# Kernel optimization log

Hardware: AMD Instinct MI355X
Metric: run time of the kernel (lower is better)

Reference implementation:

```python
import jax, jax.numpy as jnp
import numpy as np

TAU_MEM = 20.0          # tau for both ExpLeak (syn) and LIF (mem)
SPIKE_THRESHOLD = 1.0
WIDTH_GRAD = 0.5        # surrogate gradient width (unused in fwd)
SCALE_GRAD = 1.0


def setup_inputs() -> dict:
    key = jax.random.key(0)
    k1, k2 = jax.random.split(key)
    x = jax.random.normal(k1, (32, 2048, 512, 1), dtype=jnp.float32)
    weight = jax.random.uniform(k2, (1, 1), dtype=jnp.float32)  # Linear(1,1,bias=False) weight (set to scalar `weight` in torch)
    return {"x": x, "weight": weight}


def reference(x, weight):
    # x: (B, T, N, 1); weight: (1, 1)
    alpha = jnp.exp(jnp.asarray(-1.0 / TAU_MEM, dtype=x.dtype))
    i_in = x * weight[0, 0]                      # Linear(1,1,no bias)
    i_in = jnp.moveaxis(i_in, 1, 0)              # (T, B, N, 1) for scan over time

    def step(carry, i_t):
        v_syn, v_mem = carry
        # ExpLeak, norm_input=False: v_syn = alpha*v_syn + input
        v_syn = alpha * v_syn + i_t
        # LIF, norm_input=False: decay then integrate synaptic current
        v_mem = alpha * v_mem + v_syn
        # SingleSpike: at most one spike per step
        spk = (v_mem >= SPIKE_THRESHOLD).astype(v_mem.dtype)
        # MembraneSubtract reset
        v_mem = v_mem - SPIKE_THRESHOLD * spk
        return (v_syn, v_mem), spk

    zeros = jnp.zeros_like(i_in[0])
    _, spikes = jax.lax.scan(step, (zeros, zeros), i_in)
    return jnp.moveaxis(spikes, 0, 1)            # (B, T, N, 1)
```

## Files before the change

### kernel.cpp

```cpp
#include <hip/hip_runtime.h>
#include <math.h>


constexpr int B_ = 32;
constexpr int T_ = 2048;
constexpr int N_ = 512;
constexpr int TILE = 32;
constexpr int NT = T_ / TILE;

__global__ __launch_bounds__(64, 1)
void exodus_direct_kernel(const float* __restrict__ x,
                          const float* __restrict__ wptr,
                          float* __restrict__ out) {
    const int blk  = blockIdx.x;
    const int b    = blk >> 3;
    const int n0   = (blk & 7) * 64;
    const int lane = threadIdx.x;

    const size_t base = (size_t)b * T_ * N_ + (size_t)n0 + lane;
    const float* __restrict__ xp = x + base;
    float* __restrict__ op = out + base;

    const float w = wptr[0];
    const float alpha = (float)exp((double)(-1.0f / 20.0f));

    float bufA[TILE], bufB[TILE];

#pragma unroll
    for (int i = 0; i < TILE; ++i) bufA[i] = xp[(size_t)i * N_];

    float vsyn = 0.0f, vmem = 0.0f;

    for (int t = 0; t < NT; t += 2) {
        {
            const float* __restrict__ g = xp + (size_t)(t + 1) * TILE * N_;
#pragma unroll
            for (int i = 0; i < TILE; ++i) bufB[i] = g[(size_t)i * N_];
        }
        {
            float* __restrict__ o = op + (size_t)t * TILE * N_;
#pragma unroll
            for (int j = 0; j < TILE; ++j) {
                const float i_t = __fmul_rn(bufA[j], w);
                vsyn = __fadd_rn(__fmul_rn(alpha, vsyn), i_t);
                const float va = __fadd_rn(__fmul_rn(alpha, vmem), vsyn);
                const bool fire = (va >= 1.0f);
                __builtin_nontemporal_store(fire ? 1.0f : 0.0f,
                                            o + (size_t)j * N_);
                vmem = fire ? __fsub_rn(va, 1.0f) : va;
            }
        }
        if (t + 2 < NT) {
            const float* __restrict__ g = xp + (size_t)(t + 2) * TILE * N_;
#pragma unroll
            for (int i = 0; i < TILE; ++i) bufA[i] = g[(size_t)i * N_];
        }
        {
            float* __restrict__ o = op + (size_t)(t + 1) * TILE * N_;
#pragma unroll
            for (int j = 0; j < TILE; ++j) {
                const float i_t = __fmul_rn(bufB[j], w);
                vsyn = __fadd_rn(__fmul_rn(alpha, vsyn), i_t);
                const float va = __fadd_rn(__fmul_rn(alpha, vmem), vsyn);
                const bool fire = (va >= 1.0f);
                __builtin_nontemporal_store(fire ? 1.0f : 0.0f,
                                            o + (size_t)j * N_);
                vmem = fire ? __fsub_rn(va, 1.0f) : va;
            }
        }
    }
}

extern "C" void kernel_launch(void* const* d_in, const int* in_sizes, int n_in,
                              void* d_out, int out_size, void* d_ws, size_t ws_size,
                              hipStream_t stream) {
    const float* x = (const float*)d_in[0];
    const float* w = (const float*)d_in[1];
    float* out = (float*)d_out;

    dim3 grid(256);
    dim3 block(64);
    hipLaunchKernelGGL(exodus_direct_kernel, grid, block, 0, stream, x, w, out);
}
```

Baseline: 258.6 us.

## Hand-schedule loads and stores with inline asm and four-deep tile prefetch

Replaces the compiler-generated double-buffered loop with inline-asm global loads and stores that use a scalar base plus lane offset. Four input tile buffers keep two tiles of prefetch in flight, and explicit s_waitcnt vmcnt counts with sched barriers control how much memory traffic stays outstanding. This targets memory latency stalls in the sequential scan, where only 256 single-wave blocks run. The cost is higher register pressure, fragile manual waitcnt accounting, and stores that are no longer nontemporal.

```diff
diff --git a/kernel.cpp b/kernel.cpp
--- a/kernel.cpp
+++ b/kernel.cpp
@@ -2,73 +2,95 @@
 #include <math.h>
 
 
-constexpr int B_ = 32;
 constexpr int T_ = 2048;
 constexpr int N_ = 512;
 constexpr int TILE = 32;
 constexpr int NT = T_ / TILE;
 
+#define GLOADTILE(BUF, TT)                                                   \
+  {                                                                          \
+    const float* gp_ = xq + (size_t)(TT) * TILE * N_;                        \
+    _Pragma("unroll")                                                        \
+    for (int i_ = 0; i_ < TILE; ++i_) {                                      \
+      asm volatile("global_load_dword %0, %1, %2"                            \
+                   : "=v"(BUF[i_])                                           \
+                   : "v"(voff), "s"(gp_ + (size_t)i_ * N_));                 \
+    }                                                                        \
+  }
+
+#define COMPUTE(BUF, SPK, TT)                                                \
+  {                                                                          \
+    const float* op_ = oq + (size_t)(TT) * TILE * N_;                        \
+    _Pragma("unroll")                                                        \
+    for (int j_ = 0; j_ < TILE; ++j_) {                                      \
+      const float it_ = __fmul_rn(BUF[j_], w);                               \
+      vsyn = __fadd_rn(__fmul_rn(alpha, vsyn), it_);                         \
+      const float va_ = __fadd_rn(__fmul_rn(alpha, vmem), vsyn);             \
+      const bool fire_ = (va_ >= 1.0f);                                      \
+      SPK[j_] = fire_ ? 1.0f : 0.0f;                                         \
+      asm volatile("global_store_dword %1, %0, %2"                           \
+                   :: "v"(SPK[j_]), "v"(voff),                               \
+                      "s"(op_ + (size_t)j_ * N_)                             \
+                   : "memory");                                              \
+      vmem = fire_ ? __fsub_rn(va_, 1.0f) : va_;                             \
+    }                                                                        \
+  }
+
+#define KEEPALIVE16(S, O)                                                    \
+  asm volatile("" :: "v"(S[(O)+0]),  "v"(S[(O)+1]),  "v"(S[(O)+2]),          \
+                     "v"(S[(O)+3]),  "v"(S[(O)+4]),  "v"(S[(O)+5]),          \
+                     "v"(S[(O)+6]),  "v"(S[(O)+7]),  "v"(S[(O)+8]),          \
+                     "v"(S[(O)+9]),  "v"(S[(O)+10]), "v"(S[(O)+11]),         \
+                     "v"(S[(O)+12]), "v"(S[(O)+13]), "v"(S[(O)+14]),         \
+                     "v"(S[(O)+15]))
+
+#define SUBSTEP(BUFC, SPKC, SPKP, BUFP, TT, DOPF)                            \
+  {                                                                          \
+    COMPUTE(BUFC, SPKC, TT);                                                 \
+    asm volatile("s_waitcnt vmcnt(32)");                                     \
+    __builtin_amdgcn_sched_barrier(0);                                       \
+    KEEPALIVE16(SPKP, 0);                                                    \
+    KEEPALIVE16(SPKP, 16);                                                   \
+    if (DOPF) { GLOADTILE(BUFP, (TT) + 2); }                                 \
+  }
+
 __global__ __launch_bounds__(64, 1)
-void exodus_direct_kernel(const float* __restrict__ x,
-                          const float* __restrict__ wptr,
-                          float* __restrict__ out) {
+void exodus_asm_kernel(const float* __restrict__ x,
+                       const float* __restrict__ wptr,
+                       float* __restrict__ out) {
     const int blk  = blockIdx.x;
     const int b    = blk >> 3;
     const int n0   = (blk & 7) * 64;
     const int lane = threadIdx.x;
 
-    const size_t base = (size_t)b * T_ * N_ + (size_t)n0 + lane;
-    const float* __restrict__ xp = x + base;
-    float* __restrict__ op = out + base;
+    const float* __restrict__ xq  = x   + (size_t)b * T_ * N_ + n0;
+    float*       __restrict__ oq  = out + (size_t)b * T_ * N_ + n0;
+    const unsigned voff = (unsigned)lane * 4u;
 
     const float w = wptr[0];
     const float alpha = (float)exp((double)(-1.0f / 20.0f));
-
-    float bufA[TILE], bufB[TILE];
-
-#pragma unroll
-    for (int i = 0; i < TILE; ++i) bufA[i] = xp[(size_t)i * N_];
-
     float vsyn = 0.0f, vmem = 0.0f;
 
-    for (int t = 0; t < NT; t += 2) {
-        {
-            const float* __restrict__ g = xp + (size_t)(t + 1) * TILE * N_;
+    float B0[TILE], B1[TILE], B2[TILE], B3[TILE];
+    float s0[TILE], s1[TILE];
 #pragma unroll
-            for (int i = 0; i < TILE; ++i) bufB[i] = g[(size_t)i * N_];
-        }
-        {
-            float* __restrict__ o = op + (size_t)t * TILE * N_;
-#pragma unroll
-            for (int j = 0; j < TILE; ++j) {
-                const float i_t = __fmul_rn(bufA[j], w);
-                vsyn = __fadd_rn(__fmul_rn(alpha, vsyn), i_t);
-                const float va = __fadd_rn(__fmul_rn(alpha, vmem), vsyn);
-                const bool fire = (va >= 1.0f);
-                __builtin_nontemporal_store(fire ? 1.0f : 0.0f,
-                                            o + (size_t)j * N_);
-                vmem = fire ? __fsub_rn(va, 1.0f) : va;
-            }
-        }
-        if (t + 2 < NT) {
-            const float* __restrict__ g = xp + (size_t)(t + 2) * TILE * N_;
-#pragma unroll
-            for (int i = 0; i < TILE; ++i) bufA[i] = g[(size_t)i * N_];
-        }
-        {
-            float* __restrict__ o = op + (size_t)(t + 1) * TILE * N_;
-#pragma unroll
-            for (int j = 0; j < TILE; ++j) {
-                const float i_t = __fmul_rn(bufB[j], w);
-                vsyn = __fadd_rn(__fmul_rn(alpha, vsyn), i_t);
-                const float va = __fadd_rn(__fmul_rn(alpha, vmem), vsyn);
-                const bool fire = (va >= 1.0f);
-                __builtin_nontemporal_store(fire ? 1.0f : 0.0f,
-                                            o + (size_t)j * N_);
-                vmem = fire ? __fsub_rn(va, 1.0f) : va;
-            }
-        }
+    for (int j = 0; j < TILE; ++j) { s0[j] = 0.0f; s1[j] = 0.0f; }
+
+    GLOADTILE(B0, 0);
+    GLOADTILE(B1, 1);
+    asm volatile("s_waitcnt vmcnt(32)");
+    __builtin_amdgcn_sched_barrier(0);
+
+    for (int t = 0; t < NT - 4; t += 4) {
+        SUBSTEP(B0, s0, s1, B2, t + 0, true);
+        SUBSTEP(B1, s1, s0, B3, t + 1, true);
+        SUBSTEP(B2, s0, s1, B0, t + 2, true);
+        SUBSTEP(B3, s1, s0, B1, t + 3, true);
     }
+    SUBSTEP(B0, s0, s1, B2, NT - 4, true);
+    SUBSTEP(B1, s1, s0, B3, NT - 3, true);
+    SUBSTEP(B2, s0, s1, B0, NT - 2, false);
+    SUBSTEP(B3, s1, s0, B1, NT - 1, false);
 }
 
 extern "C" void kernel_launch(void* const* d_in, const int* in_sizes, int n_in,
@@ -80,5 +102,5 @@
 
     dim3 grid(256);
     dim3 block(64);
-    hipLaunchKernelGGL(exodus_direct_kernel, grid, block, 0, stream, x, w, out);
+    hipLaunchKernelGGL(exodus_asm_kernel, grid, block, 0, stream, x, w, out);
 }
```

After: 253.2 us. -2.1%, faster.

## Deepen register prefetch pipeline to four tiles with sched barriers

Applied to the files above, without the earlier changes.

Replaces the two-buffer register double-buffering with a four-buffer ring, keeping two tiles of loads in flight ahead of the serial recurrence. Inserts scheduler barriers so the compiler cannot reorder or sink the loads past the compute blocks. The aim is to hide global-memory latency in this latency-bound kernel, which runs one wave per block and has low occupancy. In exchange it raises VGPR use to about 128 buffer registers, and the barriers constrain instruction scheduling.

```diff
diff --git a/kernel.cpp b/kernel.cpp
--- a/kernel.cpp
+++ b/kernel.cpp
@@ -2,16 +2,39 @@
 #include <math.h>
 
 
-constexpr int B_ = 32;
 constexpr int T_ = 2048;
 constexpr int N_ = 512;
 constexpr int TILE = 32;
 constexpr int NT = T_ / TILE;
 
+#define SB() __builtin_amdgcn_sched_barrier(0)
+
+#define LOADTILE(BUF, TT)                                                    \
+  {                                                                          \
+    const float* __restrict__ g_ = xp + (size_t)(TT) * TILE * N_;            \
+    _Pragma("unroll")                                                        \
+    for (int i_ = 0; i_ < TILE; ++i_) BUF[i_] = g_[(size_t)i_ * N_];         \
+  }
+
+#define COMPUTETILE(BUF, TT)                                                 \
+  {                                                                          \
+    float* __restrict__ o_ = op + (size_t)(TT) * TILE * N_;                  \
+    _Pragma("unroll")                                                        \
+    for (int j_ = 0; j_ < TILE; ++j_) {                                      \
+      const float it_ = __fmul_rn(BUF[j_], w);                               \
+      vsyn = __fadd_rn(__fmul_rn(alpha, vsyn), it_);                         \
+      const float va_ = __fadd_rn(__fmul_rn(alpha, vmem), vsyn);             \
+      const bool fire_ = (va_ >= 1.0f);                                      \
+      __builtin_nontemporal_store(fire_ ? 1.0f : 0.0f,                       \
+                                  o_ + (size_t)j_ * N_);                     \
+      vmem = fire_ ? __fsub_rn(va_, 1.0f) : va_;                             \
+    }                                                                        \
+  }
+
 __global__ __launch_bounds__(64, 1)
-void exodus_direct_kernel(const float* __restrict__ x,
-                          const float* __restrict__ wptr,
-                          float* __restrict__ out) {
+void exodus_pipe_kernel(const float* __restrict__ x,
+                        const float* __restrict__ wptr,
+                        float* __restrict__ out) {
     const int blk  = blockIdx.x;
     const int b    = blk >> 3;
     const int n0   = (blk & 7) * 64;
@@ -23,51 +46,32 @@
 
     const float w = wptr[0];
     const float alpha = (float)exp((double)(-1.0f / 20.0f));
-
-    float bufA[TILE], bufB[TILE];
-
-#pragma unroll
-    for (int i = 0; i < TILE; ++i) bufA[i] = xp[(size_t)i * N_];
-
     float vsyn = 0.0f, vmem = 0.0f;
 
-    for (int t = 0; t < NT; t += 2) {
-        {
-            const float* __restrict__ g = xp + (size_t)(t + 1) * TILE * N_;
-#pragma unroll
-            for (int i = 0; i < TILE; ++i) bufB[i] = g[(size_t)i * N_];
-        }
-        {
-            float* __restrict__ o = op + (size_t)t * TILE * N_;
-#pragma unroll
-            for (int j = 0; j < TILE; ++j) {
-                const float i_t = __fmul_rn(bufA[j], w);
-                vsyn = __fadd_rn(__fmul_rn(alpha, vsyn), i_t);
-                const float va = __fadd_rn(__fmul_rn(alpha, vmem), vsyn);
-                const bool fire = (va >= 1.0f);
-                __builtin_nontemporal_store(fire ? 1.0f : 0.0f,
-                                            o + (size_t)j * N_);
-                vmem = fire ? __fsub_rn(va, 1.0f) : va;
-            }
-        }
-        if (t + 2 < NT) {
-            const float* __restrict__ g = xp + (size_t)(t + 2) * TILE * N_;
-#pragma unroll
-            for (int i = 0; i < TILE; ++i) bufA[i] = g[(size_t)i * N_];
-        }
-        {
-            float* __restrict__ o = op + (size_t)(t + 1) * TILE * N_;
-#pragma unroll
-            for (int j = 0; j < TILE; ++j) {
-                const float i_t = __fmul_rn(bufB[j], w);
-                vsyn = __fadd_rn(__fmul_rn(alpha, vsyn), i_t);
-                const float va = __fadd_rn(__fmul_rn(alpha, vmem), vsyn);
-                const bool fire = (va >= 1.0f);
-                __builtin_nontemporal_store(fire ? 1.0f : 0.0f,
-                                            o + (size_t)j * N_);
-                vmem = fire ? __fsub_rn(va, 1.0f) : va;
-            }
-        }
+    float B0[TILE], B1[TILE], B2[TILE], B3[TILE];
+
+    LOADTILE(B0, 0);
+    SB();
+    LOADTILE(B1, 1);
+    SB();
+
+    for (int t = 0; t < NT; t += 4) {
+        LOADTILE(B2, t + 2);
+        SB();
+        COMPUTETILE(B0, t + 0);
+        SB();
+        LOADTILE(B3, t + 3);
+        SB();
+        COMPUTETILE(B1, t + 1);
+        SB();
+        if (t + 4 < NT) { LOADTILE(B0, t + 4); }
+        SB();
+        COMPUTETILE(B2, t + 2);
+        SB();
+        if (t + 5 < NT) { LOADTILE(B1, t + 5); }
+        SB();
+        COMPUTETILE(B3, t + 3);
+        SB();
     }
 }
 
@@ -80,5 +84,5 @@
 
     dim3 grid(256);
     dim3 block(64);
-    hipLaunchKernelGGL(exodus_direct_kernel, grid, block, 0, stream, x, w, out);
+    hipLaunchKernelGGL(exodus_pipe_kernel, grid, block, 0, stream, x, w, out);
 }
```

After: 246.5 us. 4.7% less time.

## Use producer wave with global_load_lds DMA into double-buffered LDS

Applied to the files above, without the earlier changes.

Splits each block into a producer wave that streams input tiles directly into double-buffered shared memory via global_load_lds, and a consumer wave that runs the sequential scan and writes spikes. The aim is to hide global load latency behind the serial recurrence without spending registers on prefetch buffers, and the tile grows to 64 timesteps. In exchange it adds a block barrier per tile and an LDS read pass, and with only 256 blocks the kernel stays latency-bound by the serial scan.

```diff
diff --git a/kernel.cpp b/kernel.cpp
--- a/kernel.cpp
+++ b/kernel.cpp
@@ -2,46 +2,83 @@
 #include <math.h>
 
 
-constexpr int B_ = 32;
 constexpr int T_ = 2048;
 constexpr int N_ = 512;
-constexpr int TILE = 32;
-constexpr int NT = T_ / TILE;
+constexpr int TILE = 64;
+constexpr int NTILE = T_ / TILE;
+constexpr int NCH = 64;
 
-__global__ __launch_bounds__(64, 1)
-void exodus_direct_kernel(const float* __restrict__ x,
-                          const float* __restrict__ wptr,
-                          float* __restrict__ out) {
+typedef const __attribute__((address_space(1))) void* gas_ptr;
+typedef __attribute__((address_space(3))) void* las_ptr;
+
+__global__ __launch_bounds__(128, 1)
+void exodus_dma_kernel(const float* __restrict__ x,
+                       const float* __restrict__ wptr,
+                       float* __restrict__ out) {
+    __shared__ float XBUF[2][TILE][NCH];
+
     const int blk  = blockIdx.x;
     const int b    = blk >> 3;
-    const int n0   = (blk & 7) * 64;
-    const int lane = threadIdx.x;
+    const int n0   = (blk & 7) * NCH;
+    const int wave = threadIdx.x >> 6;
+    const int lane = threadIdx.x & 63;
 
     const size_t base = (size_t)b * T_ * N_ + (size_t)n0 + lane;
-    const float* __restrict__ xp = x + base;
-    float* __restrict__ op = out + base;
 
-    const float w = wptr[0];
-    const float alpha = (float)exp((double)(-1.0f / 20.0f));
+    if (wave == 1) {
+        const float* __restrict__ xp = x + base;
 
-    float bufA[TILE], bufB[TILE];
+        {
+            const float* __restrict__ g = xp;
+#pragma unroll
+            for (int j = 0; j < TILE; ++j) {
+                __builtin_amdgcn_global_load_lds(
+                    (gas_ptr)(g + (size_t)j * N_),
+                    (las_ptr)&XBUF[0][j][0], 4, 0, 0);
+            }
+        }
+        __builtin_amdgcn_sched_barrier(0);
+        asm volatile("s_waitcnt vmcnt(0)");
+        __builtin_amdgcn_sched_barrier(0);
+        __builtin_amdgcn_s_barrier();
 
+        for (int t = 0; t < NTILE; ++t) {
+            if (t + 1 < NTILE) {
+                const float* __restrict__ g =
+                    xp + (size_t)(t + 1) * TILE * N_;
+                const int bb = (t + 1) & 1;
 #pragma unroll
-    for (int i = 0; i < TILE; ++i) bufA[i] = xp[(size_t)i * N_];
+                for (int j = 0; j < TILE; ++j) {
+                    __builtin_amdgcn_global_load_lds(
+                        (gas_ptr)(g + (size_t)j * N_),
+                        (las_ptr)&XBUF[bb][j][0], 4, 0, 0);
+                }
+                __builtin_amdgcn_sched_barrier(0);
+                asm volatile("s_waitcnt vmcnt(0)");
+                __builtin_amdgcn_sched_barrier(0);
+            }
+            __builtin_amdgcn_s_barrier();
+        }
+    } else {
+        float* __restrict__ op = out + base;
+        const float w = wptr[0];
+        const float alpha = (float)exp((double)(-1.0f / 20.0f));
+        float vsyn = 0.0f, vmem = 0.0f;
 
-    float vsyn = 0.0f, vmem = 0.0f;
+        __builtin_amdgcn_s_barrier();
 
-    for (int t = 0; t < NT; t += 2) {
-        {
-            const float* __restrict__ g = xp + (size_t)(t + 1) * TILE * N_;
+        for (int t = 0; t < NTILE; ++t) {
+            const int bb = t & 1;
+            __builtin_amdgcn_sched_barrier(0);
+
+            float xv[TILE];
 #pragma unroll
-            for (int i = 0; i < TILE; ++i) bufB[i] = g[(size_t)i * N_];
-        }
-        {
+            for (int j = 0; j < TILE; ++j) xv[j] = XBUF[bb][j][lane];
+
             float* __restrict__ o = op + (size_t)t * TILE * N_;
 #pragma unroll
             for (int j = 0; j < TILE; ++j) {
-                const float i_t = __fmul_rn(bufA[j], w);
+                const float i_t = __fmul_rn(xv[j], w);
                 vsyn = __fadd_rn(__fmul_rn(alpha, vsyn), i_t);
                 const float va = __fadd_rn(__fmul_rn(alpha, vmem), vsyn);
                 const bool fire = (va >= 1.0f);
@@ -49,24 +86,8 @@
                                             o + (size_t)j * N_);
                 vmem = fire ? __fsub_rn(va, 1.0f) : va;
             }
-        }
-        if (t + 2 < NT) {
-            const float* __restrict__ g = xp + (size_t)(t + 2) * TILE * N_;
-#pragma unroll
-            for (int i = 0; i < TILE; ++i) bufA[i] = g[(size_t)i * N_];
-        }
-        {
-            float* __restrict__ o = op + (size_t)(t + 1) * TILE * N_;
-#pragma unroll
-            for (int j = 0; j < TILE; ++j) {
-                const float i_t = __fmul_rn(bufB[j], w);
-                vsyn = __fadd_rn(__fmul_rn(alpha, vsyn), i_t);
-                const float va = __fadd_rn(__fmul_rn(alpha, vmem), vsyn);
-                const bool fire = (va >= 1.0f);
-                __builtin_nontemporal_store(fire ? 1.0f : 0.0f,
-                                            o + (size_t)j * N_);
-                vmem = fire ? __fsub_rn(va, 1.0f) : va;
-            }
+            __builtin_amdgcn_sched_barrier(0);
+            __builtin_amdgcn_s_barrier();
         }
     }
 }
@@ -79,6 +100,6 @@
     float* out = (float*)d_out;
 
     dim3 grid(256);
-    dim3 block(64);
-    hipLaunchKernelGGL(exodus_direct_kernel, grid, block, 0, stream, x, w, out);
+    dim3 block(128);
+    hipLaunchKernelGGL(exodus_dma_kernel, grid, block, 0, stream, x, w, out);
 }
```

New measurement: 239.2 us. 7.5% less time.
